# Performance work log

Hardware: AMD Instinct MI355X
Metric: run time of the kernel (lower is better)

Reference implementation:

```python
import jax, jax.numpy as jnp
import numpy as np
from jax import lax

EPS = 1e-8  # torch F.cosine_similarity default eps


def setup_inputs() -> dict:
    key = jax.random.key(0)
    k1, k2, k3 = jax.random.split(key, 3)
    B, S, D_in, D_out, W = 256, 10, 4096, 4096, 5
    x = jax.random.normal(k1, (B, S, D_in), dtype=jnp.float32)
    # Conv1d weight [out_channels, in_channels, kernel] with PyTorch-style init scale
    fan_in = D_in * W
    conv_w = jax.random.normal(k2, (D_out, D_in, W), dtype=jnp.float32) / np.sqrt(fan_in)
    conv_b = jax.random.normal(k3, (D_out,), dtype=jnp.float32) / np.sqrt(fan_in)
    return {"x": x, "conv_w": conv_w, "conv_b": conv_b}


def _cosine_weight(x):
    # x: [B, S, D]; central frame index = S//2 + 1 (as in the original code)
    S = x.shape[1]
    c = S // 2 + 1
    central = x[:, c, :]                               # [B, D]
    dots = jnp.einsum("bsd,bd->bs", x, central)        # [B, S]
    norms = jnp.sqrt(jnp.sum(x * x, axis=-1))          # [B, S]
    cnorm = norms[:, c]                                # [B]
    denom = jnp.maximum(norms, EPS) * jnp.maximum(cnorm, EPS)[:, None]
    w = dots / denom                                   # [B, S] (raw weights; normalization in source is dead code)
    return x * w[..., None]                            # [B, S, D]


def reference(x, conv_w, conv_b):
    xw = _cosine_weight(x)                             # [B, S, D_in]
    xc = jnp.transpose(xw, (0, 2, 1))                  # [B, D_in, S]
    y = lax.conv_general_dilated(
        xc, conv_w, window_strides=(1,), padding="VALID",
        dimension_numbers=("NCH", "OIH", "NCH"),
    )                                                  # [B, D_out, S-W+1]
    y = y + conv_b[None, :, None]
    return jnp.mean(y, axis=-1)                        # [B, D_out]
```

## Files before the change

kernel.cpp:

```cpp
#include <hip/hip_runtime.h>
#include <hip/hip_bf16.h>

typedef __hip_bfloat16 bf16;
typedef __attribute__((ext_vector_type(8))) __bf16 bf16x8;
typedef __attribute__((ext_vector_type(4))) float f32x4;

typedef const __attribute__((address_space(1))) void cgvoid;
typedef __attribute__((address_space(3))) void lvoid;

constexpr int B_ = 256, S_ = 10, D_ = 4096, W_ = 5;
constexpr int K_ = D_ * W_;
constexpr int M_ = 256, N_ = 4096;
constexpr int KS_ = 16;
constexpr int KPER = K_ / KS_;
constexpr int BK_ = 32;
constexpr int ITERS = KPER / BK_;
constexpr float EPSV = 1e-8f;

__global__ void detect_kernel(const unsigned short* __restrict__ xr, int* __restrict__ flag){
    int lane = threadIdx.x;
    int sane = 0;
    for (int i = lane; i < 2048; i += 64){
        unsigned short u = xr[i];
        int e = (u >> 7) & 0xFF;
        if ((e >= 97 && e <= 137) || ((u & 0x7FFF) == 0)) sane++;
    }
    #pragma unroll
    for (int off = 32; off > 0; off >>= 1) sane += __shfl_down(sane, off);
    if (lane == 0) *flag = (sane >= 1536) ? 1 : 0;
}

__global__ __launch_bounds__(512) void zw_kernel(const void* __restrict__ xv,
                                                 bf16* __restrict__ Z,
                                                 const int* __restrict__ flag){
    const bool isb = (*flag != 0);
    int b = blockIdx.x, t = threadIdx.x;
    int i0 = t * 8;
    float f[S_][8];
    if (isb){
        const __bf16* xb = (const __bf16*)xv + (size_t)b * S_ * D_ + i0;
        #pragma unroll
        for (int s = 0; s < S_; ++s){
            bf16x8 v = *(const bf16x8*)(xb + s * D_);
            #pragma unroll
            for (int j = 0; j < 8; ++j) f[s][j] = (float)v[j];
        }
    } else {
        const float* xb = (const float*)xv + (size_t)b * S_ * D_ + i0;
        #pragma unroll
        for (int s = 0; s < S_; ++s){
            float4 a = *(const float4*)(xb + s * D_);
            float4 c = *(const float4*)(xb + s * D_ + 4);
            f[s][0]=a.x; f[s][1]=a.y; f[s][2]=a.z; f[s][3]=a.w;
            f[s][4]=c.x; f[s][5]=c.y; f[s][6]=c.z; f[s][7]=c.w;
        }
    }
    float dsum[S_], nsum[S_];
    #pragma unroll
    for (int s = 0; s < S_; ++s){
        float d = 0.f, n = 0.f;
        #pragma unroll
        for (int j = 0; j < 8; ++j){ d += f[s][j] * f[6][j]; n += f[s][j] * f[s][j]; }
        dsum[s] = d; nsum[s] = n;
    }
    int lane = t & 63, wv = t >> 6;
    #pragma unroll
    for (int s = 0; s < S_; ++s){
        #pragma unroll
        for (int off = 32; off > 0; off >>= 1){
            dsum[s] += __shfl_down(dsum[s], off);
            nsum[s] += __shfl_down(nsum[s], off);
        }
    }
    __shared__ float sd[8][S_], sn[8][S_], wsh[S_];
    if (lane == 0){
        #pragma unroll
        for (int s = 0; s < S_; ++s){ sd[wv][s] = dsum[s]; sn[wv][s] = nsum[s]; }
    }
    __syncthreads();
    if (t < S_){
        float Dv = 0.f, Nv = 0.f;
        #pragma unroll
        for (int w2 = 0; w2 < 8; ++w2){ Dv += sd[w2][t]; Nv += sn[w2][t]; }
        sd[0][t] = Dv; sn[0][t] = sqrtf(Nv);
    }
    __syncthreads();
    if (t < S_){
        wsh[t] = sd[0][t] / (fmaxf(sn[0][t], EPSV) * fmaxf(sn[0][6], EPSV));
    }
    __syncthreads();
    float w_[S_];
    #pragma unroll
    for (int s = 0; s < S_; ++s) w_[s] = wsh[s];
    alignas(16) __bf16 zout[40];
    #pragma unroll
    for (int k = 0; k < W_; ++k){
        #pragma unroll
        for (int j = 0; j < 8; ++j){
            float acc = 0.f;
            #pragma unroll
            for (int t2 = 0; t2 < 6; ++t2) acc += w_[k + t2] * f[k + t2][j];
            zout[j * 5 + k] = (__bf16)acc;
        }
    }
    __bf16* zp = (__bf16*)Z + (size_t)b * K_ + (size_t)i0 * W_;
    #pragma unroll
    for (int v = 0; v < 5; ++v) *(bf16x8*)(zp + v * 8) = *(const bf16x8*)(zout + v * 8);
}

__global__ __launch_bounds__(512, 2) void gemm_kernel(const void* __restrict__ Wv,
                                                      const bf16* __restrict__ A,
                                                      float* __restrict__ P,
                                                      const int* __restrict__ flag){
    __shared__ alignas(16) __bf16 As[256 * BK_];
    __shared__ alignas(16) __bf16 Bs[128 * BK_];
    const bool isb = (*flag != 0);
    int tid = threadIdx.x, bid = blockIdx.x;
    int nt = bid & 31, ks = bid >> 5;
    int lane = tid & 63, wv = tid >> 6;
    int wm = wv & 3, wn = wv >> 2;
    int r16 = lane & 15, quad = lane >> 4;

    const __bf16* Ab = (const __bf16*)A + (size_t)ks * KPER;

    f32x4 acc[4][4];
    #pragma unroll
    for (int fm = 0; fm < 4; ++fm)
        #pragma unroll
        for (int fn = 0; fn < 4; ++fn) acc[fm][fn] = (f32x4){0.f, 0.f, 0.f, 0.f};

    for (int kk = 0; kk < ITERS; ++kk){
        int k0 = kk * BK_;
        __syncthreads();
        #pragma unroll
        for (int r = 0; r < 2; ++r){
            int c = r * 512 + tid;
            const __bf16* src = Ab + (size_t)(c >> 2) * K_ + (c & 3) * 8 + k0;
            __builtin_amdgcn_global_load_lds((cgvoid*)src, (lvoid*)(As + c * 8), 16, 0, 0);
        }
        if (isb){
            const __bf16* Bb = (const __bf16*)Wv + (size_t)(nt * 128) * K_ + (size_t)ks * KPER;
            const __bf16* src = Bb + (size_t)(tid >> 2) * K_ + (tid & 3) * 8 + k0;
            __builtin_amdgcn_global_load_lds((cgvoid*)src, (lvoid*)(Bs + tid * 8), 16, 0, 0);
        } else {
            const float* Bb = (const float*)Wv + (size_t)(nt * 128) * K_ + (size_t)ks * KPER;
            const float* src = Bb + (size_t)(tid >> 2) * K_ + (tid & 3) * 8 + k0;
            float4 f0 = *(const float4*)src;
            float4 f1 = *(const float4*)(src + 4);
            bf16x8 u;
            u[0] = (__bf16)f0.x; u[1] = (__bf16)f0.y; u[2] = (__bf16)f0.z; u[3] = (__bf16)f0.w;
            u[4] = (__bf16)f1.x; u[5] = (__bf16)f1.y; u[6] = (__bf16)f1.z; u[7] = (__bf16)f1.w;
            *(bf16x8*)(Bs + (tid >> 2) * BK_ + (tid & 3) * 8) = u;
        }
        __syncthreads();
        bf16x8 af[4], bfr[4];
        #pragma unroll
        for (int fm = 0; fm < 4; ++fm)
            af[fm] = *(const bf16x8*)(As + (wm * 64 + fm * 16 + r16) * BK_ + quad * 8);
        #pragma unroll
        for (int fn = 0; fn < 4; ++fn)
            bfr[fn] = *(const bf16x8*)(Bs + (wn * 64 + fn * 16 + r16) * BK_ + quad * 8);
        #pragma unroll
        for (int fm = 0; fm < 4; ++fm)
            #pragma unroll
            for (int fn = 0; fn < 4; ++fn)
                acc[fm][fn] = __builtin_amdgcn_mfma_f32_16x16x32_bf16(af[fm], bfr[fn], acc[fm][fn], 0, 0, 0);
    }

    float* Pb = P + (size_t)ks * M_ * N_;
    #pragma unroll
    for (int fm = 0; fm < 4; ++fm){
        #pragma unroll
        for (int fn = 0; fn < 4; ++fn){
            int n = nt * 128 + wn * 64 + fn * 16 + r16;
            #pragma unroll
            for (int r = 0; r < 4; ++r){
                int m = wm * 64 + fm * 16 + quad * 4 + r;
                Pb[(size_t)m * N_ + n] = acc[fm][fn][r];
            }
        }
    }
}

__global__ __launch_bounds__(256) void reduce_kernel(const float* __restrict__ P,
                                                     const void* __restrict__ bias,
                                                     void* __restrict__ out,
                                                     const int* __restrict__ flag){
    const bool isb = (*flag != 0);
    int gid = blockIdx.x * 256 + threadIdx.x;
    int o4 = gid * 4;
    int n = o4 & (N_ - 1);
    float4 s = make_float4(0.f, 0.f, 0.f, 0.f);
    #pragma unroll
    for (int k2 = 0; k2 < KS_; ++k2){
        float4 p = *(const float4*)(P + (size_t)k2 * M_ * N_ + o4);
        s.x += p.x; s.y += p.y; s.z += p.z; s.w += p.w;
    }
    const float inv6 = 1.f / 6.f;
    float b0, b1, b2, b3;
    if (isb){
        const bf16* bp = (const bf16*)bias + n;
        b0 = __bfloat162float(bp[0]); b1 = __bfloat162float(bp[1]);
        b2 = __bfloat162float(bp[2]); b3 = __bfloat162float(bp[3]);
    } else {
        const float* bp = (const float*)bias + n;
        b0 = bp[0]; b1 = bp[1]; b2 = bp[2]; b3 = bp[3];
    }
    float r0 = s.x * inv6 + b0;
    float r1 = s.y * inv6 + b1;
    float r2 = s.z * inv6 + b2;
    float r3 = s.w * inv6 + b3;
    if (isb){
        bf16 h0 = __float2bfloat16(r0), h1 = __float2bfloat16(r1);
        bf16 h2 = __float2bfloat16(r2), h3 = __float2bfloat16(r3);
        ushort4 o;
        o.x = *(unsigned short*)&h0; o.y = *(unsigned short*)&h1;
        o.z = *(unsigned short*)&h2; o.w = *(unsigned short*)&h3;
        *(ushort4*)((unsigned short*)out + o4) = o;
    } else {
        *(float4*)((float*)out + o4) = make_float4(r0, r1, r2, r3);
    }
}

extern "C" void kernel_launch(void* const* d_in, const int* in_sizes, int n_in,
                              void* d_out, int out_size, void* d_ws, size_t ws_size,
                              hipStream_t stream){
    const void* x      = d_in[0];
    const void* conv_w = d_in[1];
    const void* conv_b = d_in[2];

    char* ws   = (char*)d_ws;
    int*  flag = (int*)ws;
    bf16* Z    = (bf16*)(ws + 16384);
    float* P   = (float*)(ws + 10502144);

    detect_kernel<<<1, 64, 0, stream>>>((const unsigned short*)x, flag);
    zw_kernel<<<256, 512, 0, stream>>>(x, Z, flag);
    gemm_kernel<<<512, 512, 0, stream>>>(conv_w, Z, P, flag);
    reduce_kernel<<<1024, 256, 0, stream>>>(P, conv_b, d_out, flag);
}
```

Before: 514.7 us.

## Double-buffer GEMM shared-memory tiles and halve split-K factor

The GEMM kernel gets two LDS buffers for the A and B tiles, so the loads for the next K step are issued before the MFMA work on the current step and one barrier per iteration is removed. In the fp32-weight path the float loads stay in registers during the MFMAs and are converted to bf16 afterwards. The split-K factor drops from 16 to 8, which halves the grid and the partial-sum traffic to the reduce kernel. In exchange each block runs a longer K loop, the GPU runs fewer concurrent blocks, and LDS use and register pressure go up.

```diff
diff --git a/kernel.cpp b/kernel.cpp
--- a/kernel.cpp
+++ b/kernel.cpp
@@ -11,7 +11,7 @@
 constexpr int B_ = 256, S_ = 10, D_ = 4096, W_ = 5;
 constexpr int K_ = D_ * W_;
 constexpr int M_ = 256, N_ = 4096;
-constexpr int KS_ = 16;
+constexpr int KS_ = 8;
 constexpr int KPER = K_ / KS_;
 constexpr int BK_ = 32;
 constexpr int ITERS = KPER / BK_;
@@ -112,8 +112,8 @@
                                                       const bf16* __restrict__ A,
                                                       float* __restrict__ P,
                                                       const int* __restrict__ flag){
-    __shared__ alignas(16) __bf16 As[256 * BK_];
-    __shared__ alignas(16) __bf16 Bs[128 * BK_];
+    __shared__ alignas(16) __bf16 As[2][256 * BK_];
+    __shared__ alignas(16) __bf16 Bs[2][128 * BK_];
     const bool isb = (*flag != 0);
     int tid = threadIdx.x, bid = blockIdx.x;
     int nt = bid & 31, ks = bid >> 5;
@@ -121,7 +121,9 @@
     int wm = wv & 3, wn = wv >> 2;
     int r16 = lane & 15, quad = lane >> 4;
 
-    const __bf16* Ab = (const __bf16*)A + (size_t)ks * KPER;
+    const __bf16* Ab   = (const __bf16*)A + (size_t)ks * KPER;
+    const __bf16* Bb_b = (const __bf16*)Wv + (size_t)(nt * 128) * K_ + (size_t)ks * KPER;
+    const float*  Bb_f = (const float*) Wv + (size_t)(nt * 128) * K_ + (size_t)ks * KPER;
 
     f32x4 acc[4][4];
     #pragma unroll
@@ -129,42 +131,67 @@
         #pragma unroll
         for (int fn = 0; fn < 4; ++fn) acc[fm][fn] = (f32x4){0.f, 0.f, 0.f, 0.f};
 
+    #pragma unroll
+    for (int r = 0; r < 2; ++r){
+        int c = r * 512 + tid;
+        const __bf16* src = Ab + (size_t)(c >> 2) * K_ + (c & 3) * 8;
+        __builtin_amdgcn_global_load_lds((cgvoid*)src, (lvoid*)(&As[0][0] + c * 8), 16, 0, 0);
+    }
+    if (isb){
+        const __bf16* src = Bb_b + (size_t)(tid >> 2) * K_ + (tid & 3) * 8;
+        __builtin_amdgcn_global_load_lds((cgvoid*)src, (lvoid*)(&Bs[0][0] + tid * 8), 16, 0, 0);
+    } else {
+        const float* src = Bb_f + (size_t)(tid >> 2) * K_ + (tid & 3) * 8;
+        float4 f0 = *(const float4*)src;
+        float4 f1 = *(const float4*)(src + 4);
+        bf16x8 u;
+        u[0] = (__bf16)f0.x; u[1] = (__bf16)f0.y; u[2] = (__bf16)f0.z; u[3] = (__bf16)f0.w;
+        u[4] = (__bf16)f1.x; u[5] = (__bf16)f1.y; u[6] = (__bf16)f1.z; u[7] = (__bf16)f1.w;
+        *(bf16x8*)(&Bs[0][(tid >> 2) * BK_ + (tid & 3) * 8]) = u;
+    }
+    __syncthreads();
+
+    #pragma unroll 2
     for (int kk = 0; kk < ITERS; ++kk){
-        int k0 = kk * BK_;
-        __syncthreads();
-        #pragma unroll
-        for (int r = 0; r < 2; ++r){
-            int c = r * 512 + tid;
-            const __bf16* src = Ab + (size_t)(c >> 2) * K_ + (c & 3) * 8 + k0;
-            __builtin_amdgcn_global_load_lds((cgvoid*)src, (lvoid*)(As + c * 8), 16, 0, 0);
-        }
-        if (isb){
-            const __bf16* Bb = (const __bf16*)Wv + (size_t)(nt * 128) * K_ + (size_t)ks * KPER;
-            const __bf16* src = Bb + (size_t)(tid >> 2) * K_ + (tid & 3) * 8 + k0;
-            __builtin_amdgcn_global_load_lds((cgvoid*)src, (lvoid*)(Bs + tid * 8), 16, 0, 0);
-        } else {
-            const float* Bb = (const float*)Wv + (size_t)(nt * 128) * K_ + (size_t)ks * KPER;
-            const float* src = Bb + (size_t)(tid >> 2) * K_ + (tid & 3) * 8 + k0;
-            float4 f0 = *(const float4*)src;
-            float4 f1 = *(const float4*)(src + 4);
+        int cur = kk & 1, nxt = cur ^ 1;
+        bool havenext = (kk + 1 < ITERS);
+        float4 f0, f1;
+        if (havenext){
+            int kn = (kk + 1) * BK_;
+            #pragma unroll
+            for (int r = 0; r < 2; ++r){
+                int c = r * 512 + tid;
+                const __bf16* src = Ab + (size_t)(c >> 2) * K_ + (c & 3) * 8 + kn;
+                __builtin_amdgcn_global_load_lds((cgvoid*)src, (lvoid*)(&As[nxt][0] + c * 8), 16, 0, 0);
+            }
+            if (isb){
+                const __bf16* src = Bb_b + (size_t)(tid >> 2) * K_ + (tid & 3) * 8 + kn;
+                __builtin_amdgcn_global_load_lds((cgvoid*)src, (lvoid*)(&Bs[nxt][0] + tid * 8), 16, 0, 0);
+            } else {
+                const float* src = Bb_f + (size_t)(tid >> 2) * K_ + (tid & 3) * 8 + kn;
+                f0 = *(const float4*)src;
+                f1 = *(const float4*)(src + 4);
+            }
+        }
+        bf16x8 af[4], bfr[4];
+        #pragma unroll
+        for (int fm = 0; fm < 4; ++fm)
+            af[fm] = *(const bf16x8*)(&As[cur][(wm * 64 + fm * 16 + r16) * BK_ + quad * 8]);
+        #pragma unroll
+        for (int fn = 0; fn < 4; ++fn)
+            bfr[fn] = *(const bf16x8*)(&Bs[cur][(wn * 64 + fn * 16 + r16) * BK_ + quad * 8]);
+        #pragma unroll
+        for (int fm = 0; fm < 4; ++fm)
+            #pragma unroll
+            for (int fn = 0; fn < 4; ++fn)
+                acc[fm][fn] = __builtin_amdgcn_mfma_f32_16x16x32_bf16(af[fm], bfr[fn], acc[fm][fn], 0, 0, 0);
+        if (havenext && !isb){
             bf16x8 u;
             u[0] = (__bf16)f0.x; u[1] = (__bf16)f0.y; u[2] = (__bf16)f0.z; u[3] = (__bf16)f0.w;
             u[4] = (__bf16)f1.x; u[5] = (__bf16)f1.y; u[6] = (__bf16)f1.z; u[7] = (__bf16)f1.w;
-            *(bf16x8*)(Bs + (tid >> 2) * BK_ + (tid & 3) * 8) = u;
+            *(bf16x8*)(&Bs[nxt][(tid >> 2) * BK_ + (tid & 3) * 8]) = u;
         }
         __syncthreads();
-        bf16x8 af[4], bfr[4];
-        #pragma unroll
-        for (int fm = 0; fm < 4; ++fm)
-            af[fm] = *(const bf16x8*)(As + (wm * 64 + fm * 16 + r16) * BK_ + quad * 8);
-        #pragma unroll
-        for (int fn = 0; fn < 4; ++fn)
-            bfr[fn] = *(const bf16x8*)(Bs + (wn * 64 + fn * 16 + r16) * BK_ + quad * 8);
-        #pragma unroll
-        for (int fm = 0; fm < 4; ++fm)
-            #pragma unroll
-            for (int fn = 0; fn < 4; ++fn)
-                acc[fm][fn] = __builtin_amdgcn_mfma_f32_16x16x32_bf16(af[fm], bfr[fn], acc[fm][fn], 0, 0, 0);
     }
 
     float* Pb = P + (size_t)ks * M_ * N_;
@@ -236,6 +263,6 @@
 
     detect_kernel<<<1, 64, 0, stream>>>((const unsigned short*)x, flag);
     zw_kernel<<<256, 512, 0, stream>>>(x, Z, flag);
-    gemm_kernel<<<512, 512, 0, stream>>>(conv_w, Z, P, flag);
+    gemm_kernel<<<256, 512, 0, stream>>>(conv_w, Z, P, flag);
     reduce_kernel<<<1024, 256, 0, stream>>>(P, conv_b, d_out, flag);
 }
```

New measurement: 524.3 us. Within noise of the previous version (+1.9%).
